# Optimization experiments

Hardware: AMD Instinct MI355X
Metric: run time of the kernel (lower is better)

Reference implementation:

```python
import jax, jax.numpy as jnp
import numpy as np
import math

N_GENES_TOTAL = 5000   # full gene table (fragments.n_genes)
N_CELLS_TOTAL = 10000  # full cell count (libsize buffer)
NBINS = 128            # spline components per gene
N_LATENT = 64
B = 256                # n_cells in minibatch
G = 2000               # genes_oi
NCUTS = 500_000


def setup_inputs() -> dict:
    key = jax.random.key(0)
    ks = jax.random.split(key, 12)
    latent = jax.random.normal(ks[0], (B, N_LATENT), jnp.float32)
    genes_oi = jax.random.randint(ks[1], (G,), 0, N_GENES_TOTAL)
    cells_oi = jax.random.randint(ks[2], (B,), 0, N_CELLS_TOTAL)
    cut_coordinates = jax.random.uniform(ks[3], (NCUTS,), jnp.float32)
    cut_local_cellxgene_ix = jax.random.randint(ks[4], (NCUTS,), 0, B * G)
    cut_local_gene_ix = jax.random.randint(ks[5], (NCUTS,), 0, G)
    local_cellxgene_ix = jax.random.randint(ks[6], (NCUTS,), 0, B * G)
    s = 1.0 / math.sqrt(N_LATENT)
    logit_weight = jax.random.uniform(ks[7], (N_GENES_TOTAL, N_LATENT, NBINS), jnp.float32, -s, s)
    rho_weight = jax.random.uniform(ks[8], (N_GENES_TOTAL, N_LATENT), jnp.float32, -s / 100.0, s / 100.0)
    rho_bias = jax.random.uniform(ks[9], (N_GENES_TOTAL,), jnp.float32, 1e-4, 1e-2)
    libsize = jax.random.randint(ks[10], (N_CELLS_TOTAL,), 1000, 20000)
    spline_heights = 0.01 * jax.random.normal(ks[11], (N_GENES_TOTAL, NBINS), jnp.float32)
    return {
        "latent": latent, "genes_oi": genes_oi, "cells_oi": cells_oi,
        "cut_coordinates": cut_coordinates,
        "cut_local_cellxgene_ix": cut_local_cellxgene_ix,
        "cut_local_gene_ix": cut_local_gene_ix,
        "local_cellxgene_ix": local_cellxgene_ix,
        "logit_weight": logit_weight, "rho_weight": rho_weight,
        "rho_bias": rho_bias, "libsize": libsize,
        "spline_heights": spline_heights,
        "n_cells": B, "n_genes": G,
    }


def reference(latent, genes_oi, cells_oi, cut_coordinates,
              cut_local_cellxgene_ix, cut_local_gene_ix, local_cellxgene_ix,
              logit_weight, rho_weight, rho_bias, libsize, spline_heights,
              n_cells, n_genes):
    # Decoder with n_layers=0: nn is identity
    lw = logit_weight[genes_oi]                     # [G, L, C]
    rw = rho_weight[genes_oi]                       # [G, L]
    mixture_delta = jnp.einsum('bl,glc->bgc', latent, lw)   # [B, G, C]
    rho_delta = latent @ rw.T                       # [B, G]

    # gather per-cut mixture deltas
    delta_flat = mixture_delta.reshape(n_cells * n_genes, -1)
    delta_cut = delta_flat[cut_local_cellxgene_ix]  # [Ncuts, C]

    # spline/mixture log-likelihood: per-gene histogram density with delta
    gene_heights = spline_heights[genes_oi]         # [G, C]
    h = gene_heights[cut_local_gene_ix] + delta_cut  # [Ncuts, C]
    logp_bins = jax.nn.log_softmax(h, axis=-1)
    nbins = h.shape[-1]
    bin_ix = jnp.clip((cut_coordinates * nbins).astype(jnp.int32), 0, nbins - 1)
    likelihood_mixture = (
        jnp.take_along_axis(logp_bins, bin_ix[:, None], axis=-1)[:, 0]
        + jnp.log(jnp.float32(nbins))
    )

    # Poisson fragment-count likelihood
    rate = (rho_bias[genes_oi][None, :] * jnp.exp(rho_delta)
            * libsize[cells_oi].astype(jnp.float32)[:, None])   # [B, G]
    counts = jnp.bincount(local_cellxgene_ix, length=n_cells * n_genes)
    counts = counts.reshape(n_cells, n_genes).astype(jnp.float32)
    ll_counts = counts * jnp.log(rate) - rate - jax.scipy.special.gammaln(counts + 1.0)

    likelihood = likelihood_mixture.sum() + ll_counts.sum()
    return -likelihood
```

## Files before the change

kernel.cpp:

```cpp
#include <hip/hip_runtime.h>

#define LDIM 64
#define CDIM 128
#define NREP 16
#define SUBCAP 32
#define MAXPER (NREP * SUBCAP)
#define LOG128 4.8520302639196171f

typedef __attribute__((ext_vector_type(8))) short bfrag;
typedef __attribute__((ext_vector_type(4))) float f32x4;

static __device__ __forceinline__ unsigned short f2bf(float f) {
    unsigned int x = __float_as_uint(f);
    unsigned int r = (x + 0x7fffu + ((x >> 16) & 1u)) >> 16;
    return (unsigned short)r;
}
static __device__ __forceinline__ float bf2f(unsigned int u) {
    return __uint_as_float(u << 16);
}

__global__ __launch_bounds__(256) void zero_kernel(uint4* __restrict__ p, size_t n16,
                                                   float* __restrict__ out, int out_size) {
    size_t i = (size_t)blockIdx.x * blockDim.x + threadIdx.x;
    size_t stride = (size_t)gridDim.x * blockDim.x;
    for (; i < n16; i += stride) p[i] = make_uint4(0u, 0u, 0u, 0u);
    if (blockIdx.x == 0 && threadIdx.x < (unsigned)out_size) out[threadIdx.x] = 0.f;
}

__global__ __launch_bounds__(256) void prep1_kernel(
    const float* __restrict__ heights, unsigned short* __restrict__ hbf, int nheights,
    const float* __restrict__ latent, unsigned short* __restrict__ latbf, int nlat,
    const int* __restrict__ cut_pair, const int* __restrict__ cut_gene,
    const float* __restrict__ coord, const int* __restrict__ genes_oi,
    const int* __restrict__ local_cxg, unsigned int* __restrict__ cnt_rep,
    unsigned int* __restrict__ bucket, unsigned int* __restrict__ countsT,
    int ncuts, int B, int G, int N, unsigned int magicG) {
    int stride = gridDim.x * blockDim.x;
    int rep = blockIdx.x & (NREP - 1);
    int nb = 2 * G;
    for (int i = blockIdx.x * blockDim.x + threadIdx.x; i < N; i += stride) {
        if (i < nheights) hbf[i] = f2bf(heights[i]);
        if (i < nlat) latbf[i] = f2bf(latent[i]);
        if (i < ncuts) {
            unsigned int p = (unsigned int)cut_pair[i];
            unsigned int cell = __umulhi(p, magicG);
            unsigned int g = p - cell * (unsigned int)G;
            unsigned int gg = (unsigned int)genes_oi[cut_gene[i]];
            int bin = (int)(coord[i] * 128.0f);
            bin = min(max(bin, 0), 127);
            unsigned int bidx = g * 2u + (cell >> 7);
            unsigned int slot = atomicAdd(&cnt_rep[rep * nb + (int)bidx], 1u);
            if (slot < SUBCAP)
                bucket[(size_t)bidx * MAXPER + rep * SUBCAP + slot] =
                    (cell << 24) | (gg << 7) | (unsigned int)bin;
            unsigned int q = (unsigned int)local_cxg[i];
            unsigned int cell2 = __umulhi(q, magicG);
            unsigned int g2 = q - cell2 * (unsigned int)G;
            atomicAdd(&countsT[(size_t)g2 * (unsigned int)B + cell2], 1u);
        }
    }
}

__global__ __launch_bounds__(512, 6) void fused_kernel(
    const float* __restrict__ latent, const unsigned short* __restrict__ latbf,
    const int* __restrict__ genes_oi, const float* __restrict__ logit_weight,
    const unsigned short* __restrict__ hbf, const unsigned int* __restrict__ bucket,
    const unsigned int* __restrict__ cnt_rep, const unsigned int* __restrict__ countsT,
    const int* __restrict__ cells_oi,
    const float* __restrict__ rho_weight, const float* __restrict__ rho_bias,
    const int* __restrict__ libsize, int B, int G, float* __restrict__ out) {
    __shared__ unsigned short dlds[128 * CDIM];
    __shared__ unsigned short blds[CDIM * LDIM];
    __shared__ unsigned int clds[MAXPER];
    __shared__ float red[8];
    int t = threadIdx.x;
    int bid = blockIdx.x;
    int g = bid >> 1, half = bid & 1;
    int gene = genes_oi[g];
    int nb = 2 * G;
    int wv = t >> 6, ln = t & 63;
    int l15 = ln & 15, l4 = ln >> 4;
    float accs = 0.f;

    int n = t & 127;
    int k0 = (t >> 7) * 16;
    const float* src = logit_weight + (size_t)gene * LDIM * CDIM;
    float wv_[16];
    #pragma unroll
    for (int j = 0; j < 16; ++j) wv_[j] = src[(size_t)(k0 + j) * CDIM + n];
    bfrag a_[2];
    #pragma unroll
    for (int ks = 0; ks < 2; ++ks)
        a_[ks] = *(const bfrag*)(latbf + (half * 128 + wv * 16 + l15) * LDIM + ks * 32 + l4 * 8);

    unsigned int cs[NREP + 1];
    cs[0] = 0;
    #pragma unroll
    for (int r = 0; r < NREP; ++r)
        cs[r + 1] = cs[r] + min(cnt_rep[r * nb + bid], (unsigned)SUBCAP);

    if (t < 128) {
        int cell = half * 128 + t;
        const float4* la = (const float4*)(latent + (size_t)cell * LDIM);
        const float4* rw = (const float4*)(rho_weight + (size_t)gene * LDIM);
        float d = 0.f;
        #pragma unroll
        for (int k = 0; k < LDIM / 4; ++k) {
            float4 a = la[k], w = rw[k];
            d += a.x * w.x + a.y * w.y + a.z * w.z + a.w * w.w;
        }
        float rb = rho_bias[gene];
        float lib = (float)libsize[cells_oi[cell]];
        float lrate = __logf(rb) + d + __logf(lib);
        float rate = __expf(lrate);
        unsigned int c = countsT[(size_t)g * B + cell];
        float lgam = 0.f;
        for (unsigned int k = 2; k <= c; ++k) lgam += __logf((float)k);
        accs += (float)c * lrate - rate - lgam;
    }

    {
        const unsigned int* bk = bucket + (size_t)bid * MAXPER;
        #pragma unroll
        for (int r = 0; r < NREP; ++r) {
            unsigned int base = cs[r], cr = cs[r + 1] - base;
            for (unsigned int i = (unsigned int)t; i < cr; i += 512u)
                clds[base + i] = bk[r * SUBCAP + i];
        }
    }

    {
        #pragma unroll
        for (int h = 0; h < 2; ++h) {
            union { unsigned short u[8]; uint4 q; } pk;
            #pragma unroll
            for (int j = 0; j < 8; ++j) pk.u[j] = f2bf(wv_[h * 8 + j]);
            int kk = k0 + h * 8;
            *(uint4*)(blds + n * LDIM + (kk ^ ((n & 7) * 8))) = pk.q;
        }
    }
    __syncthreads();

    f32x4 acc[8];
    #pragma unroll
    for (int q = 0; q < 8; ++q) acc[q] = (f32x4){0.f, 0.f, 0.f, 0.f};
    #pragma unroll
    for (int ks = 0; ks < 2; ++ks) {
        int kk = ks * 32 + l4 * 8;
        #pragma unroll
        for (int q = 0; q < 8; ++q) {
            int col = q * 16 + l15;
            bfrag b = *(const bfrag*)(blds + col * LDIM + (kk ^ ((col & 7) * 8)));
            acc[q] = __builtin_amdgcn_mfma_f32_16x16x32_bf16(a_[ks], b, acc[q], 0, 0, 0);
        }
    }
    #pragma unroll
    for (int q = 0; q < 8; ++q)
        #pragma unroll
        for (int r = 0; r < 4; ++r) {
            int row = wv * 16 + l4 * 4 + r;
            int col = q * 16 + l15;
            dlds[row * CDIM + (col ^ ((row & 7) * 8))] = f2bf(acc[q][r]);
        }
    __syncthreads();

    {
        unsigned int C = cs[NREP];
        int grp = t >> 3, sub = t & 7;
        for (unsigned int i = (unsigned int)grp; i < C; i += 64u) {
            unsigned int rc = clds[i];
            int row = (int)((rc >> 24) & 127u);
            unsigned int gg = (rc >> 7) & 0x1FFFu;
            int sw = (row & 7) * 8;
            uint4 dva = *(const uint4*)(dlds + row * CDIM + ((sub * 16) ^ sw));
            uint4 dvb = *(const uint4*)(dlds + row * CDIM + ((sub * 16 + 8) ^ sw));
            const uint4* hp = (const uint4*)(hbf + ((size_t)gg << 7) + sub * 16);
            uint4 hva = hp[0], hvb = hp[1];
            float h0  = bf2f(hva.x & 0xffffu) + bf2f(dva.x & 0xffffu);
            float h1  = bf2f(hva.x >> 16)     + bf2f(dva.x >> 16);
            float h2  = bf2f(hva.y & 0xffffu) + bf2f(dva.y & 0xffffu);
            float h3  = bf2f(hva.y >> 16)     + bf2f(dva.y >> 16);
            float h4  = bf2f(hva.z & 0xffffu) + bf2f(dva.z & 0xffffu);
            float h5  = bf2f(hva.z >> 16)     + bf2f(dva.z >> 16);
            float h6  = bf2f(hva.w & 0xffffu) + bf2f(dva.w & 0xffffu);
            float h7  = bf2f(hva.w >> 16)     + bf2f(dva.w >> 16);
            float h8  = bf2f(hvb.x & 0xffffu) + bf2f(dvb.x & 0xffffu);
            float h9  = bf2f(hvb.x >> 16)     + bf2f(dvb.x >> 16);
            float h10 = bf2f(hvb.y & 0xffffu) + bf2f(dvb.y & 0xffffu);
            float h11 = bf2f(hvb.y >> 16)     + bf2f(dvb.y >> 16);
            float h12 = bf2f(hvb.z & 0xffffu) + bf2f(dvb.z & 0xffffu);
            float h13 = bf2f(hvb.z >> 16)     + bf2f(dvb.z >> 16);
            float h14 = bf2f(hvb.w & 0xffffu) + bf2f(dvb.w & 0xffffu);
            float h15 = bf2f(hvb.w >> 16)     + bf2f(dvb.w >> 16);
            float s = __expf(h0)  + __expf(h1)  + __expf(h2)  + __expf(h3)
                    + __expf(h4)  + __expf(h5)  + __expf(h6)  + __expf(h7)
                    + __expf(h8)  + __expf(h9)  + __expf(h10) + __expf(h11)
                    + __expf(h12) + __expf(h13) + __expf(h14) + __expf(h15);
            #pragma unroll
            for (int o = 1; o < 8; o <<= 1) s += __shfl_xor(s, o);
            int bin = (int)(rc & 127u);
            int e = bin & 15;
            float sel = h0;
            sel = (e == 1)  ? h1  : sel;
            sel = (e == 2)  ? h2  : sel;
            sel = (e == 3)  ? h3  : sel;
            sel = (e == 4)  ? h4  : sel;
            sel = (e == 5)  ? h5  : sel;
            sel = (e == 6)  ? h6  : sel;
            sel = (e == 7)  ? h7  : sel;
            sel = (e == 8)  ? h8  : sel;
            sel = (e == 9)  ? h9  : sel;
            sel = (e == 10) ? h10 : sel;
            sel = (e == 11) ? h11 : sel;
            sel = (e == 12) ? h12 : sel;
            sel = (e == 13) ? h13 : sel;
            sel = (e == 14) ? h14 : sel;
            sel = (e == 15) ? h15 : sel;
            float hsel = __shfl(sel, (ln & 56) | (bin >> 4));
            if (sub == 0) accs += hsel - __logf(s) + LOG128;
        }
    }

    #pragma unroll
    for (int o = 32; o; o >>= 1) accs += __shfl_xor(accs, o);
    if (ln == 0) red[wv] = accs;
    __syncthreads();
    if (t == 0) {
        float s = red[0] + red[1] + red[2] + red[3] + red[4] + red[5] + red[6] + red[7];
        atomicAdd(out, -s);
    }
}

extern "C" void kernel_launch(void* const* d_in, const int* in_sizes, int n_in,
                              void* d_out, int out_size, void* d_ws, size_t ws_size,
                              hipStream_t stream) {
    const float* latent         = (const float*)d_in[0];
    const int*   genes_oi       = (const int*)d_in[1];
    const int*   cells_oi       = (const int*)d_in[2];
    const float* cut_coord      = (const float*)d_in[3];
    const int*   cut_pair       = (const int*)d_in[4];
    const int*   cut_gene       = (const int*)d_in[5];
    const int*   local_cxg      = (const int*)d_in[6];
    const float* logit_weight   = (const float*)d_in[7];
    const float* rho_weight     = (const float*)d_in[8];
    const float* rho_bias       = (const float*)d_in[9];
    const int*   libsize        = (const int*)d_in[10];
    const float* spline_heights = (const float*)d_in[11];
    int G = in_sizes[1];
    int B = in_sizes[2];
    int ncuts = in_sizes[4];
    int nheights = in_sizes[11];
    int nlat = B * LDIM;
    unsigned int magicG = (unsigned int)((0x100000000ULL + (unsigned)G - 1) / (unsigned)G);

    char* ws = (char*)d_ws;
    size_t off = 0;
    unsigned int* countsT = (unsigned int*)(ws + off);
    off += ((size_t)B * G * 4 + 255) & ~(size_t)255;
    unsigned int* cnt_rep = (unsigned int*)(ws + off);
    off += ((size_t)2 * G * NREP * 4 + 255) & ~(size_t)255;
    size_t zero_bytes = off;
    unsigned int* bucket = (unsigned int*)(ws + off);
    off += ((size_t)2 * G * MAXPER * 4 + 255) & ~(size_t)255;
    unsigned short* hbf = (unsigned short*)(ws + off);
    off += ((size_t)nheights * 2 + 255) & ~(size_t)255;
    unsigned short* latbf = (unsigned short*)(ws + off);
    off += ((size_t)nlat * 2 + 255) & ~(size_t)255;

    float* out = (float*)d_out;
    zero_kernel<<<1024, 256, 0, stream>>>((uint4*)ws, zero_bytes / 16, out, out_size);

    int N = ncuts > nheights ? ncuts : nheights;
    prep1_kernel<<<2048, 256, 0, stream>>>(
        spline_heights, hbf, nheights, latent, latbf, nlat,
        cut_pair, cut_gene, cut_coord, genes_oi, local_cxg,
        cnt_rep, bucket, countsT, ncuts, B, G, N, magicG);
    fused_kernel<<<2 * G, 512, 0, stream>>>(
        latent, latbf, genes_oi, logit_weight, hbf, bucket,
        cnt_rep, countsT, cells_oi,
        rho_weight, rho_bias, libsize, B, G, out);
}
```

Baseline: 144.9 us.

## Process one gene per block and pre-transpose logit weights to bf16

The fused kernel now handles all 256 cells of a gene in one block instead of splitting cells across two blocks. This halves the per-gene logit-weight reads and bucket bookkeeping. A new prep2 kernel transposes and converts each selected gene's logit weights to bf16 in workspace, so the MFMA B operand is read directly from global memory instead of being staged through LDS. The cost is an extra kernel launch and a bf16 round-trip through global memory. LDS use per block doubles for the delta tile, and the bucket replication is reshaped (fewer replicas with larger capacity), which changes atomic contention and the per-bucket overflow limits.

```diff
diff --git a/kernel.cpp b/kernel.cpp
--- a/kernel.cpp
+++ b/kernel.cpp
@@ -2,8 +2,8 @@
 
 #define LDIM 64
 #define CDIM 128
-#define NREP 16
-#define SUBCAP 32
+#define NREP 8
+#define SUBCAP 64
 #define MAXPER (NREP * SUBCAP)
 #define LOG128 4.8520302639196171f
 
@@ -37,7 +37,6 @@
     int ncuts, int B, int G, int N, unsigned int magicG) {
     int stride = gridDim.x * blockDim.x;
     int rep = blockIdx.x & (NREP - 1);
-    int nb = 2 * G;
     for (int i = blockIdx.x * blockDim.x + threadIdx.x; i < N; i += stride) {
         if (i < nheights) hbf[i] = f2bf(heights[i]);
         if (i < nlat) latbf[i] = f2bf(latent[i]);
@@ -48,10 +47,9 @@
             unsigned int gg = (unsigned int)genes_oi[cut_gene[i]];
             int bin = (int)(coord[i] * 128.0f);
             bin = min(max(bin, 0), 127);
-            unsigned int bidx = g * 2u + (cell >> 7);
-            unsigned int slot = atomicAdd(&cnt_rep[rep * nb + (int)bidx], 1u);
+            unsigned int slot = atomicAdd(&cnt_rep[rep * G + (int)g], 1u);
             if (slot < SUBCAP)
-                bucket[(size_t)bidx * MAXPER + rep * SUBCAP + slot] =
+                bucket[(size_t)g * MAXPER + rep * SUBCAP + slot] =
                     (cell << 24) | (gg << 7) | (unsigned int)bin;
             unsigned int q = (unsigned int)local_cxg[i];
             unsigned int cell2 = __umulhi(q, magicG);
@@ -61,66 +59,59 @@
     }
 }
 
-__global__ __launch_bounds__(512, 6) void fused_kernel(
+__global__ __launch_bounds__(512) void prep2_kernel(
+    const float* __restrict__ lw, const int* __restrict__ genes_oi,
+    unsigned short* __restrict__ lwT, int G) {
+    __shared__ float s[LDIM][CDIM + 1];
+    int g = blockIdx.x, t = threadIdx.x;
+    int gene = genes_oi[g];
+    const float4* src = (const float4*)(lw + (size_t)gene * LDIM * CDIM);
+    #pragma unroll
+    for (int it = 0; it < 4; ++it) {
+        int idx = t + it * 512;
+        int k = idx >> 5, nq = idx & 31;
+        float4 v = src[idx];
+        s[k][nq * 4 + 0] = v.x; s[k][nq * 4 + 1] = v.y;
+        s[k][nq * 4 + 2] = v.z; s[k][nq * 4 + 3] = v.w;
+    }
+    __syncthreads();
+    #pragma unroll
+    for (int it = 0; it < 2; ++it) {
+        int idx = t + it * 512;
+        int n = idx >> 3, kq = idx & 7;
+        union { unsigned short u[8]; uint4 q; } pk;
+        #pragma unroll
+        for (int j = 0; j < 8; ++j) pk.u[j] = f2bf(s[kq * 8 + j][n]);
+        *(uint4*)(lwT + ((size_t)g * CDIM + n) * LDIM + kq * 8) = pk.q;
+    }
+}
+
+__global__ __launch_bounds__(512, 2) void fused_kernel(
     const float* __restrict__ latent, const unsigned short* __restrict__ latbf,
-    const int* __restrict__ genes_oi, const float* __restrict__ logit_weight,
+    const int* __restrict__ genes_oi, const unsigned short* __restrict__ lwT,
     const unsigned short* __restrict__ hbf, const unsigned int* __restrict__ bucket,
     const unsigned int* __restrict__ cnt_rep, const unsigned int* __restrict__ countsT,
     const int* __restrict__ cells_oi,
     const float* __restrict__ rho_weight, const float* __restrict__ rho_bias,
     const int* __restrict__ libsize, int B, int G, float* __restrict__ out) {
-    __shared__ unsigned short dlds[128 * CDIM];
-    __shared__ unsigned short blds[CDIM * LDIM];
+    __shared__ unsigned short dlds[256 * CDIM];
     __shared__ unsigned int clds[MAXPER];
     __shared__ float red[8];
     int t = threadIdx.x;
-    int bid = blockIdx.x;
-    int g = bid >> 1, half = bid & 1;
+    int g = blockIdx.x;
     int gene = genes_oi[g];
-    int nb = 2 * G;
     int wv = t >> 6, ln = t & 63;
     int l15 = ln & 15, l4 = ln >> 4;
     float accs = 0.f;
 
-    int n = t & 127;
-    int k0 = (t >> 7) * 16;
-    const float* src = logit_weight + (size_t)gene * LDIM * CDIM;
-    float wv_[16];
-    #pragma unroll
-    for (int j = 0; j < 16; ++j) wv_[j] = src[(size_t)(k0 + j) * CDIM + n];
-    bfrag a_[2];
-    #pragma unroll
-    for (int ks = 0; ks < 2; ++ks)
-        a_[ks] = *(const bfrag*)(latbf + (half * 128 + wv * 16 + l15) * LDIM + ks * 32 + l4 * 8);
-
     unsigned int cs[NREP + 1];
     cs[0] = 0;
     #pragma unroll
     for (int r = 0; r < NREP; ++r)
-        cs[r + 1] = cs[r] + min(cnt_rep[r * nb + bid], (unsigned)SUBCAP);
-
-    if (t < 128) {
-        int cell = half * 128 + t;
-        const float4* la = (const float4*)(latent + (size_t)cell * LDIM);
-        const float4* rw = (const float4*)(rho_weight + (size_t)gene * LDIM);
-        float d = 0.f;
-        #pragma unroll
-        for (int k = 0; k < LDIM / 4; ++k) {
-            float4 a = la[k], w = rw[k];
-            d += a.x * w.x + a.y * w.y + a.z * w.z + a.w * w.w;
-        }
-        float rb = rho_bias[gene];
-        float lib = (float)libsize[cells_oi[cell]];
-        float lrate = __logf(rb) + d + __logf(lib);
-        float rate = __expf(lrate);
-        unsigned int c = countsT[(size_t)g * B + cell];
-        float lgam = 0.f;
-        for (unsigned int k = 2; k <= c; ++k) lgam += __logf((float)k);
-        accs += (float)c * lrate - rate - lgam;
-    }
+        cs[r + 1] = cs[r] + min(cnt_rep[r * G + g], (unsigned)SUBCAP);
 
     {
-        const unsigned int* bk = bucket + (size_t)bid * MAXPER;
+        const unsigned int* bk = bucket + (size_t)g * MAXPER;
         #pragma unroll
         for (int r = 0; r < NREP; ++r) {
             unsigned int base = cs[r], cr = cs[r + 1] - base;
@@ -130,38 +121,35 @@
     }
 
     {
-        #pragma unroll
-        for (int h = 0; h < 2; ++h) {
-            union { unsigned short u[8]; uint4 q; } pk;
-            #pragma unroll
-            for (int j = 0; j < 8; ++j) pk.u[j] = f2bf(wv_[h * 8 + j]);
-            int kk = k0 + h * 8;
-            *(uint4*)(blds + n * LDIM + (kk ^ ((n & 7) * 8))) = pk.q;
-        }
-    }
-    __syncthreads();
-
-    f32x4 acc[8];
-    #pragma unroll
-    for (int q = 0; q < 8; ++q) acc[q] = (f32x4){0.f, 0.f, 0.f, 0.f};
-    #pragma unroll
-    for (int ks = 0; ks < 2; ++ks) {
-        int kk = ks * 32 + l4 * 8;
-        #pragma unroll
-        for (int q = 0; q < 8; ++q) {
-            int col = q * 16 + l15;
-            bfrag b = *(const bfrag*)(blds + col * LDIM + (kk ^ ((col & 7) * 8)));
-            acc[q] = __builtin_amdgcn_mfma_f32_16x16x32_bf16(a_[ks], b, acc[q], 0, 0, 0);
-        }
-    }
-    #pragma unroll
-    for (int q = 0; q < 8; ++q)
-        #pragma unroll
-        for (int r = 0; r < 4; ++r) {
-            int row = wv * 16 + l4 * 4 + r;
-            int col = q * 16 + l15;
-            dlds[row * CDIM + (col ^ ((row & 7) * 8))] = f2bf(acc[q][r]);
-        }
+        f32x4 acc[2][8];
+        #pragma unroll
+        for (int m = 0; m < 2; ++m)
+            #pragma unroll
+            for (int q = 0; q < 8; ++q) acc[m][q] = (f32x4){0.f, 0.f, 0.f, 0.f};
+        #pragma unroll
+        for (int ks = 0; ks < 2; ++ks) {
+            int kk = ks * 32 + l4 * 8;
+            bfrag a0 = *(const bfrag*)(latbf + (wv * 32 + l15) * LDIM + kk);
+            bfrag a1 = *(const bfrag*)(latbf + (wv * 32 + 16 + l15) * LDIM + kk);
+            #pragma unroll
+            for (int q = 0; q < 8; ++q) {
+                int col = q * 16 + l15;
+                bfrag b = *(const bfrag*)(lwT + ((size_t)g * CDIM + col) * LDIM + kk);
+                acc[0][q] = __builtin_amdgcn_mfma_f32_16x16x32_bf16(a0, b, acc[0][q], 0, 0, 0);
+                acc[1][q] = __builtin_amdgcn_mfma_f32_16x16x32_bf16(a1, b, acc[1][q], 0, 0, 0);
+            }
+        }
+        #pragma unroll
+        for (int m = 0; m < 2; ++m)
+            #pragma unroll
+            for (int q = 0; q < 8; ++q)
+                #pragma unroll
+                for (int r = 0; r < 4; ++r) {
+                    int row = wv * 32 + m * 16 + l4 * 4 + r;
+                    int col = q * 16 + l15;
+                    dlds[row * CDIM + (col ^ ((row & 7) * 8))] = f2bf(acc[m][q][r]);
+                }
+    }
     __syncthreads();
 
     {
@@ -169,7 +157,7 @@
         int grp = t >> 3, sub = t & 7;
         for (unsigned int i = (unsigned int)grp; i < C; i += 64u) {
             unsigned int rc = clds[i];
-            int row = (int)((rc >> 24) & 127u);
+            int row = (int)(rc >> 24);
             unsigned int gg = (rc >> 7) & 0x1FFFu;
             int sw = (row & 7) * 8;
             uint4 dva = *(const uint4*)(dlds + row * CDIM + ((sub * 16) ^ sw));
@@ -221,6 +209,25 @@
         }
     }
 
+    if (t < 256) {
+        const float4* la = (const float4*)(latent + (size_t)t * LDIM);
+        const float4* rw = (const float4*)(rho_weight + (size_t)gene * LDIM);
+        float d = 0.f;
+        #pragma unroll
+        for (int k = 0; k < LDIM / 4; ++k) {
+            float4 a = la[k], w = rw[k];
+            d += a.x * w.x + a.y * w.y + a.z * w.z + a.w * w.w;
+        }
+        float rb = rho_bias[gene];
+        float lib = (float)libsize[cells_oi[t]];
+        float lrate = __logf(rb) + d + __logf(lib);
+        float rate = __expf(lrate);
+        unsigned int c = countsT[(size_t)g * B + t];
+        float lgam = 0.f;
+        for (unsigned int k = 2; k <= c; ++k) lgam += __logf((float)k);
+        accs += (float)c * lrate - rate - lgam;
+    }
+
     #pragma unroll
     for (int o = 32; o; o >>= 1) accs += __shfl_xor(accs, o);
     if (ln == 0) red[wv] = accs;
@@ -258,10 +265,12 @@
     unsigned int* countsT = (unsigned int*)(ws + off);
     off += ((size_t)B * G * 4 + 255) & ~(size_t)255;
     unsigned int* cnt_rep = (unsigned int*)(ws + off);
-    off += ((size_t)2 * G * NREP * 4 + 255) & ~(size_t)255;
+    off += ((size_t)G * NREP * 4 + 255) & ~(size_t)255;
     size_t zero_bytes = off;
     unsigned int* bucket = (unsigned int*)(ws + off);
-    off += ((size_t)2 * G * MAXPER * 4 + 255) & ~(size_t)255;
+    off += ((size_t)G * MAXPER * 4 + 255) & ~(size_t)255;
+    unsigned short* lwT = (unsigned short*)(ws + off);
+    off += ((size_t)G * CDIM * LDIM * 2 + 255) & ~(size_t)255;
     unsigned short* hbf = (unsigned short*)(ws + off);
     off += ((size_t)nheights * 2 + 255) & ~(size_t)255;
     unsigned short* latbf = (unsigned short*)(ws + off);
@@ -275,8 +284,9 @@
         spline_heights, hbf, nheights, latent, latbf, nlat,
         cut_pair, cut_gene, cut_coord, genes_oi, local_cxg,
         cnt_rep, bucket, countsT, ncuts, B, G, N, magicG);
-    fused_kernel<<<2 * G, 512, 0, stream>>>(
-        latent, latbf, genes_oi, logit_weight, hbf, bucket,
+    prep2_kernel<<<G, 512, 0, stream>>>(logit_weight, genes_oi, lwT, G);
+    fused_kernel<<<G, 512, 0, stream>>>(
+        latent, latbf, genes_oi, lwT, hbf, bucket,
         cnt_rep, countsT, cells_oi,
         rho_weight, rho_bias, libsize, B, G, out);
 }
```

Result: no change. 145.3 us (+0.3%).

## Pre-transpose gathered logit weights to bf16 in a prep kernel fused with zeroing

Applied to the files above, without the earlier changes.

A new prep2 kernel gathers each selected gene's logit_weight slice, transposes it through shared memory and stores it as bf16 in a [G,128,64] workspace. The same kernel also takes over the workspace and output zeroing, so zero_kernel is removed. The fused kernel then loads MFMA operands directly from global memory instead of staging B through LDS, and it swaps the operand order so results can be packed and written to LDS as uint2. The per-cell Poisson term is moved after the mixture loop, which may help overlap latency. In exchange, each half-block reads the bf16 weights again and the extra intermediate buffer costs some global traffic.

```diff
diff --git a/kernel.cpp b/kernel.cpp
--- a/kernel.cpp
+++ b/kernel.cpp
@@ -18,13 +18,39 @@
 static __device__ __forceinline__ float bf2f(unsigned int u) {
     return __uint_as_float(u << 16);
 }
-
-__global__ __launch_bounds__(256) void zero_kernel(uint4* __restrict__ p, size_t n16,
-                                                   float* __restrict__ out, int out_size) {
-    size_t i = (size_t)blockIdx.x * blockDim.x + threadIdx.x;
-    size_t stride = (size_t)gridDim.x * blockDim.x;
-    for (; i < n16; i += stride) p[i] = make_uint4(0u, 0u, 0u, 0u);
-    if (blockIdx.x == 0 && threadIdx.x < (unsigned)out_size) out[threadIdx.x] = 0.f;
+static __device__ __forceinline__ unsigned int pack2(float hi, float lo) {
+    return (__float_as_uint(hi) & 0xffff0000u) | (__float_as_uint(lo) >> 16);
+}
+
+__global__ __launch_bounds__(512) void prep2_kernel(
+    const float* __restrict__ lw, const int* __restrict__ genes_oi,
+    unsigned short* __restrict__ lwT, uint4* __restrict__ zp, size_t zn16,
+    float* __restrict__ out, int out_size, int G) {
+    __shared__ float s[LDIM][CDIM + 1];
+    int g = blockIdx.x, t = threadIdx.x;
+    for (size_t zi = (size_t)g * 512 + t; zi < zn16; zi += (size_t)gridDim.x * 512)
+        zp[zi] = make_uint4(0u, 0u, 0u, 0u);
+    if (g == 0 && t < out_size) out[t] = 0.f;
+    int gene = genes_oi[g];
+    const float4* src = (const float4*)(lw + (size_t)gene * LDIM * CDIM);
+    #pragma unroll
+    for (int it = 0; it < 4; ++it) {
+        int idx = t + it * 512;
+        int k = idx >> 5, nq = idx & 31;
+        float4 v = src[idx];
+        s[k][nq * 4 + 0] = v.x; s[k][nq * 4 + 1] = v.y;
+        s[k][nq * 4 + 2] = v.z; s[k][nq * 4 + 3] = v.w;
+    }
+    __syncthreads();
+    #pragma unroll
+    for (int it = 0; it < 2; ++it) {
+        int idx = t + it * 512;
+        int n = idx >> 3, kq = idx & 7;
+        union { unsigned short u[8]; uint4 q; } pk;
+        #pragma unroll
+        for (int j = 0; j < 8; ++j) pk.u[j] = f2bf(s[kq * 8 + j][n]);
+        *(uint4*)(lwT + ((size_t)g * CDIM + n) * LDIM + kq * 8) = pk.q;
+    }
 }
 
 __global__ __launch_bounds__(256) void prep1_kernel(
@@ -63,14 +89,13 @@
 
 __global__ __launch_bounds__(512, 6) void fused_kernel(
     const float* __restrict__ latent, const unsigned short* __restrict__ latbf,
-    const int* __restrict__ genes_oi, const float* __restrict__ logit_weight,
+    const int* __restrict__ genes_oi, const unsigned short* __restrict__ lwT,
     const unsigned short* __restrict__ hbf, const unsigned int* __restrict__ bucket,
     const unsigned int* __restrict__ cnt_rep, const unsigned int* __restrict__ countsT,
     const int* __restrict__ cells_oi,
     const float* __restrict__ rho_weight, const float* __restrict__ rho_bias,
     const int* __restrict__ libsize, int B, int G, float* __restrict__ out) {
     __shared__ unsigned short dlds[128 * CDIM];
-    __shared__ unsigned short blds[CDIM * LDIM];
     __shared__ unsigned int clds[MAXPER];
     __shared__ float red[8];
     int t = threadIdx.x;
@@ -82,42 +107,11 @@
     int l15 = ln & 15, l4 = ln >> 4;
     float accs = 0.f;
 
-    int n = t & 127;
-    int k0 = (t >> 7) * 16;
-    const float* src = logit_weight + (size_t)gene * LDIM * CDIM;
-    float wv_[16];
-    #pragma unroll
-    for (int j = 0; j < 16; ++j) wv_[j] = src[(size_t)(k0 + j) * CDIM + n];
-    bfrag a_[2];
-    #pragma unroll
-    for (int ks = 0; ks < 2; ++ks)
-        a_[ks] = *(const bfrag*)(latbf + (half * 128 + wv * 16 + l15) * LDIM + ks * 32 + l4 * 8);
-
     unsigned int cs[NREP + 1];
     cs[0] = 0;
     #pragma unroll
     for (int r = 0; r < NREP; ++r)
         cs[r + 1] = cs[r] + min(cnt_rep[r * nb + bid], (unsigned)SUBCAP);
-
-    if (t < 128) {
-        int cell = half * 128 + t;
-        const float4* la = (const float4*)(latent + (size_t)cell * LDIM);
-        const float4* rw = (const float4*)(rho_weight + (size_t)gene * LDIM);
-        float d = 0.f;
-        #pragma unroll
-        for (int k = 0; k < LDIM / 4; ++k) {
-            float4 a = la[k], w = rw[k];
-            d += a.x * w.x + a.y * w.y + a.z * w.z + a.w * w.w;
-        }
-        float rb = rho_bias[gene];
-        float lib = (float)libsize[cells_oi[cell]];
-        float lrate = __logf(rb) + d + __logf(lib);
-        float rate = __expf(lrate);
-        unsigned int c = countsT[(size_t)g * B + cell];
-        float lgam = 0.f;
-        for (unsigned int k = 2; k <= c; ++k) lgam += __logf((float)k);
-        accs += (float)c * lrate - rate - lgam;
-    }
 
     {
         const unsigned int* bk = bucket + (size_t)bid * MAXPER;
@@ -130,38 +124,29 @@
     }
 
     {
-        #pragma unroll
-        for (int h = 0; h < 2; ++h) {
-            union { unsigned short u[8]; uint4 q; } pk;
+        f32x4 acc[8];
+        #pragma unroll
+        for (int q = 0; q < 8; ++q) acc[q] = (f32x4){0.f, 0.f, 0.f, 0.f};
+        #pragma unroll
+        for (int ks = 0; ks < 2; ++ks) {
+            int kk = ks * 32 + l4 * 8;
+            bfrag lat = *(const bfrag*)(latbf + (half * 128 + wv * 16 + l15) * LDIM + kk);
             #pragma unroll
-            for (int j = 0; j < 8; ++j) pk.u[j] = f2bf(wv_[h * 8 + j]);
-            int kk = k0 + h * 8;
-            *(uint4*)(blds + n * LDIM + (kk ^ ((n & 7) * 8))) = pk.q;
-        }
-    }
-    __syncthreads();
-
-    f32x4 acc[8];
-    #pragma unroll
-    for (int q = 0; q < 8; ++q) acc[q] = (f32x4){0.f, 0.f, 0.f, 0.f};
-    #pragma unroll
-    for (int ks = 0; ks < 2; ++ks) {
-        int kk = ks * 32 + l4 * 8;
+            for (int q = 0; q < 8; ++q) {
+                bfrag lwf = *(const bfrag*)(lwT + ((size_t)g * CDIM + q * 16 + l15) * LDIM + kk);
+                acc[q] = __builtin_amdgcn_mfma_f32_16x16x32_bf16(lwf, lat, acc[q], 0, 0, 0);
+            }
+        }
+        int cl = wv * 16 + l15;
+        int sx = (cl & 7) << 4;
         #pragma unroll
         for (int q = 0; q < 8; ++q) {
-            int col = q * 16 + l15;
-            bfrag b = *(const bfrag*)(blds + col * LDIM + (kk ^ ((col & 7) * 8)));
-            acc[q] = __builtin_amdgcn_mfma_f32_16x16x32_bf16(a_[ks], b, acc[q], 0, 0, 0);
-        }
-    }
-    #pragma unroll
-    for (int q = 0; q < 8; ++q)
-        #pragma unroll
-        for (int r = 0; r < 4; ++r) {
-            int row = wv * 16 + l4 * 4 + r;
-            int col = q * 16 + l15;
-            dlds[row * CDIM + (col ^ ((row & 7) * 8))] = f2bf(acc[q][r]);
-        }
+            unsigned int p0 = pack2(acc[q][1], acc[q][0]);
+            unsigned int p1 = pack2(acc[q][3], acc[q][2]);
+            int colx = (q * 16 + l4 * 4) ^ sx;
+            *(uint2*)(dlds + cl * CDIM + colx) = make_uint2(p0, p1);
+        }
+    }
     __syncthreads();
 
     {
@@ -171,7 +156,7 @@
             unsigned int rc = clds[i];
             int row = (int)((rc >> 24) & 127u);
             unsigned int gg = (rc >> 7) & 0x1FFFu;
-            int sw = (row & 7) * 8;
+            int sw = (row & 7) << 4;
             uint4 dva = *(const uint4*)(dlds + row * CDIM + ((sub * 16) ^ sw));
             uint4 dvb = *(const uint4*)(dlds + row * CDIM + ((sub * 16 + 8) ^ sw));
             const uint4* hp = (const uint4*)(hbf + ((size_t)gg << 7) + sub * 16);
@@ -221,6 +206,26 @@
         }
     }
 
+    if (t < 128) {
+        int cell = half * 128 + t;
+        const float4* la = (const float4*)(latent + (size_t)cell * LDIM);
+        const float4* rw = (const float4*)(rho_weight + (size_t)gene * LDIM);
+        float d = 0.f;
+        #pragma unroll
+        for (int k = 0; k < LDIM / 4; ++k) {
+            float4 a = la[k], w = rw[k];
+            d += a.x * w.x + a.y * w.y + a.z * w.z + a.w * w.w;
+        }
+        float rb = rho_bias[gene];
+        float lib = (float)libsize[cells_oi[cell]];
+        float lrate = __logf(rb) + d + __logf(lib);
+        float rate = __expf(lrate);
+        unsigned int c = countsT[(size_t)g * B + cell];
+        float lgam = 0.f;
+        for (unsigned int k = 2; k <= c; ++k) lgam += __logf((float)k);
+        accs += (float)c * lrate - rate - lgam;
+    }
+
     #pragma unroll
     for (int o = 32; o; o >>= 1) accs += __shfl_xor(accs, o);
     if (ln == 0) red[wv] = accs;
@@ -262,21 +267,23 @@
     size_t zero_bytes = off;
     unsigned int* bucket = (unsigned int*)(ws + off);
     off += ((size_t)2 * G * MAXPER * 4 + 255) & ~(size_t)255;
+    unsigned short* lwT = (unsigned short*)(ws + off);
+    off += ((size_t)G * CDIM * LDIM * 2 + 255) & ~(size_t)255;
     unsigned short* hbf = (unsigned short*)(ws + off);
     off += ((size_t)nheights * 2 + 255) & ~(size_t)255;
     unsigned short* latbf = (unsigned short*)(ws + off);
     off += ((size_t)nlat * 2 + 255) & ~(size_t)255;
 
     float* out = (float*)d_out;
-    zero_kernel<<<1024, 256, 0, stream>>>((uint4*)ws, zero_bytes / 16, out, out_size);
-
     int N = ncuts > nheights ? ncuts : nheights;
+    prep2_kernel<<<G, 512, 0, stream>>>(logit_weight, genes_oi, lwT,
+                                        (uint4*)ws, zero_bytes / 16, out, out_size, G);
     prep1_kernel<<<2048, 256, 0, stream>>>(
         spline_heights, hbf, nheights, latent, latbf, nlat,
         cut_pair, cut_gene, cut_coord, genes_oi, local_cxg,
         cnt_rep, bucket, countsT, ncuts, B, G, N, magicG);
     fused_kernel<<<2 * G, 512, 0, stream>>>(
-        latent, latbf, genes_oi, logit_weight, hbf, bucket,
+        latent, latbf, genes_oi, lwT, hbf, bucket,
         cnt_rep, countsT, cells_oi,
         rho_weight, rho_bias, libsize, B, G, out);
 }
```

Result: slower. 178.7 us (+23.4%).
